# Kernel optimization log

Measured on AMD Instinct MI355X. Metric: run time of the kernel, lower is better.

Reference implementation:

```python
import jax, jax.numpy as jnp
import numpy as np
from jax import lax

GRID_SIZE = 3
SPLINE_ORDER = 2
GRID_MIN, GRID_MAX = -1.0, 1.0
KH = KW = 4
STRIDE = 2
PAD = 1
OUT_CH = 8


def _grid():
    # extended knot vector: grid_size + 2*spline_order + 1 points over [-1,1]
    h = (GRID_MAX - GRID_MIN) / GRID_SIZE
    return (jnp.arange(-SPLINE_ORDER, GRID_SIZE + SPLINE_ORDER + 1, dtype=jnp.float32) * h
            + GRID_MIN)  # [8]


def _b_splines(x, grid):
    # x: [N, F] -> bases: [N, F, GRID_SIZE + SPLINE_ORDER] via Cox-de Boor
    x = x[..., None]  # [N, F, 1]
    bases = ((x >= grid[:-1]) & (x < grid[1:])).astype(x.dtype)
    for k in range(1, SPLINE_ORDER + 1):
        left = (x - grid[: -(k + 1)]) / (grid[k:-1] - grid[: -(k + 1)]) * bases[..., :-1]
        right = (grid[k + 1:] - x) / (grid[k + 1:] - grid[1:-k]) * bases[..., 1:]
        bases = left + right
    return bases  # [N, F, 5]


def setup_inputs() -> dict:
    key = jax.random.key(0)
    ks = jax.random.split(key, 5)
    B = 2048
    x = jax.random.normal(ks[0], (B, 3, 32, 32), dtype=jnp.float32)
    F = 3 * KH * KW  # 48
    base_weight = jax.random.normal(ks[1], (OUT_CH, F), dtype=jnp.float32) * 0.1
    spline_weight = jax.random.normal(ks[2], (OUT_CH, F, GRID_SIZE + SPLINE_ORDER), dtype=jnp.float32) * 0.1
    lin_w = jax.random.normal(ks[3], (1, OUT_CH), dtype=jnp.float32) * 0.3
    lin_b = jax.random.normal(ks[4], (1,), dtype=jnp.float32) * 0.1
    return {"x": x, "base_weight": base_weight, "spline_weight": spline_weight,
            "lin_w": lin_w, "lin_b": lin_b}


def reference(x, base_weight, spline_weight, lin_w, lin_b):
    B = x.shape[0]
    grid = _grid()
    # unfold: [B, C*KH*KW, Ho, Wo], feature order (C, kh, kw) like torch.unfold
    patches = lax.conv_general_dilated_patches(
        x, (KH, KW), (STRIDE, STRIDE), ((PAD, PAD), (PAD, PAD)))
    Bp, F, Ho, Wo = patches.shape
    p = patches.transpose(0, 2, 3, 1).reshape(-1, F)  # [B*Ho*Wo, 48]
    # KANLinear: base branch + spline branch
    base = jnp.einsum('nf,of->no', jax.nn.relu(p), base_weight)
    bas = _b_splines(p, grid)  # [N, F, 5]
    spl = jnp.einsum('nfk,ofk->no', bas, spline_weight)
    y = (base + spl).reshape(B, Ho, Wo, OUT_CH)  # conv output, channels-last
    pooled = y.mean(axis=(1, 2))  # AdaptiveAvgPool2d(1) + Flatten -> [B, 8]
    out = jax.nn.sigmoid(pooled @ lin_w.T + lin_b)  # [B, 1]
    return out
```

## Files before the change

kernel.cpp:

```cpp
#include <hip/hip_runtime.h>
#include <math.h>


__global__ __launch_bounds__(256) void kan_pixel(
    const float* __restrict__ x,
    const float* __restrict__ bw,
    const float* __restrict__ sw,
    const float* __restrict__ lw,
    const float* __restrict__ lb,
    float* __restrict__ out)
{
  __shared__ float  Spad[480];
  __shared__ float  bwcL[48];
  __shared__ float4 P[768];
  __shared__ float4 T[768];
  __shared__ float  red[4];
  __shared__ float  corrS;

  const int tid = threadIdx.x;
  const int b = blockIdx.x;

  const float4* xg = reinterpret_cast<const float4*>(x) + (size_t)b * 768;
  float4 px0 = xg[tid];
  float4 px1 = xg[tid + 256];
  float4 px2 = xg[tid + 512];

  float l[8];
  #pragma unroll
  for (int o = 0; o < 8; ++o) l[o] = lw[o];

  for (int e = tid; e < 480; e += 256) {
    int f = e / 10, m = e - f * 10;
    float v = 0.f;
    if (m >= 2 && m < 7) {
      int k = f * 5 + (m - 2);
      #pragma unroll
      for (int o = 0; o < 8; ++o) v = fmaf(l[o], sw[o * 240 + k], v);
    }
    Spad[e] = v;
  }
  if (tid < 48) {
    float v = 0.f;
    #pragma unroll
    for (int o = 0; o < 8; ++o) v = fmaf(l[o], bw[o * 48 + tid], v);
    bwcL[tid] = v;
  }
  __syncthreads();

  #pragma unroll
  for (int k = 0; k < 3; ++k) {
    int e = tid + k * 256;
    int f = e >> 4, i2 = e & 15;
    float4 r4 = make_float4(0.f, 0.f, 0.f, 0.f);
    if (i2 != 0) {
      int j2 = i2 - 1, j = j2 >> 1;
      float d = 3.5f - (float)j;
      float s0 = Spad[f * 10 + j];
      float s1 = Spad[f * 10 + j + 1];
      float s2 = Spad[f * 10 + j + 2];
      float A = 0.5f * (s0 + s1);
      float B = s1 - s0;
      float C = 0.5f * s0 - s1 + 0.5f * s2;
      r4.x = A + d * (B + d * C);
      r4.y = 1.5f * B + 3.f * d * C + (j2 >= 7 ? bwcL[f] : 0.f);
      r4.z = 2.25f * C;
    }
    P[e] = r4;
  }
  __syncthreads();

  if (tid == 0) {
    float cs = 0.f;
    for (int f = 0; f < 48; ++f) {
      int kh = (f >> 2) & 3, kw = f & 3;
      int eh = (kh == 0 || kh == 3) ? 1 : 0;
      int ew = (kw == 0 || kw == 3) ? 1 : 0;
      float n = (float)(16 * eh + 16 * ew - (eh & ew));
      cs = fmaf(n, P[f * 16 + 8].x, cs);
    }
    corrS = cs;
  }

  #pragma unroll
  for (int k = 0; k < 3; ++k) {
    int e = tid + k * 256;
    int i2 = e & 15, g = e >> 4;
    int ccl = g & 3, rc = (g >> 2) & 3, c = g >> 4;
    int khA = (0x2011 >> (rc * 4)) & 15;
    int kwA = (0x2011 >> (ccl * 4)) & 15;
    bool hB = !(rc & 1);
    bool wB = !(ccl & 1);
    int fAA = ((c * 4 + khA) * 4 + kwA) * 16 + i2;
    float4 a = P[fAA];
    if (wB)       { float4 p = P[fAA + 32];  a.x += p.x; a.y += p.y; a.z += p.z; }
    if (hB)       { float4 p = P[fAA + 128]; a.x += p.x; a.y += p.y; a.z += p.z; }
    if (hB && wB) { float4 p = P[fAA + 160]; a.x += p.x; a.y += p.y; a.z += p.z; }
    T[e] = a;
  }
  __syncthreads();

  float s = 0.f;
  auto acc1 = [&](float v, int fb) {
    float fj = floorf(fmaf(v, 3.f, 7.f));
    fj = fminf(fmaxf(fj, -1.f), 14.f);
    int i2 = (int)fj + 1;
    float4 co = T[fb + i2];
    s = fmaf(v, fmaf(v, co.z, co.y), s + co.x);
  };
  const float4 pxa[3] = {px0, px1, px2};
  #pragma unroll
  for (int i = 0; i < 3; ++i) {
    int i4 = tid + (i << 8);
    int flat = i4 << 2;
    int c = flat >> 10;
    int rem = flat & 1023;
    int r = rem >> 5;
    int col0 = rem & 31;
    int rc = ((r & 1) << 1) + (r == 0 ? 1 : 0) + (r == 31 ? 1 : 0);
    int base = (((c << 2) | rc) << 6);
    acc1(pxa[i].x, base + ((col0 == 0) ? 16 : 0));
    acc1(pxa[i].y, base + 32);
    acc1(pxa[i].z, base);
    acc1(pxa[i].w, base + ((col0 == 28) ? 48 : 32));
  }

  #pragma unroll
  for (int off = 32; off; off >>= 1) s += __shfl_down(s, off);
  if ((tid & 63) == 0) red[tid >> 6] = s;
  __syncthreads();
  if (tid == 0) {
    float tot = (red[0] + red[1]) + (red[2] + red[3]) + corrS;
    float z = tot * (1.f / 256.f) + lb[0];
    out[b] = 1.f / (1.f + expf(-z));
  }
}

extern "C" void kernel_launch(void* const* d_in, const int* in_sizes, int n_in,
                              void* d_out, int out_size, void* d_ws, size_t ws_size,
                              hipStream_t stream) {
  const float* x  = (const float*)d_in[0];
  const float* bw = (const float*)d_in[1];
  const float* sw = (const float*)d_in[2];
  const float* lw = (const float*)d_in[3];
  const float* lb = (const float*)d_in[4];
  float* out = (float*)d_out;
  int B = in_sizes[0] / 3072;
  kan_pixel<<<B, 256, 0, stream>>>(x, bw, sw, lw, lb, out);
}
```

Before: 84.02 us.

## Build weight lookup table once in separate kernel instead of per block

Result: faster. 79.47 us (-5.4%).

```diff
diff --git a/kernel.cpp b/kernel.cpp
--- a/kernel.cpp
+++ b/kernel.cpp
@@ -2,29 +2,18 @@
 #include <math.h>
 
 
-__global__ __launch_bounds__(256) void kan_pixel(
-    const float* __restrict__ x,
+__global__ __launch_bounds__(256) void kan_build(
     const float* __restrict__ bw,
     const float* __restrict__ sw,
     const float* __restrict__ lw,
-    const float* __restrict__ lb,
-    float* __restrict__ out)
+    float* __restrict__ ws)
 {
   __shared__ float  Spad[480];
   __shared__ float  bwcL[48];
   __shared__ float4 P[768];
-  __shared__ float4 T[768];
-  __shared__ float  red[4];
-  __shared__ float  corrS;
+  __shared__ float  c48[48];
 
   const int tid = threadIdx.x;
-  const int b = blockIdx.x;
-
-  const float4* xg = reinterpret_cast<const float4*>(x) + (size_t)b * 768;
-  float4 px0 = xg[tid];
-  float4 px1 = xg[tid + 256];
-  float4 px2 = xg[tid + 512];
-
   float l[8];
   #pragma unroll
   for (int o = 0; o < 8; ++o) l[o] = lw[o];
@@ -69,18 +58,15 @@
   }
   __syncthreads();
 
-  if (tid == 0) {
-    float cs = 0.f;
-    for (int f = 0; f < 48; ++f) {
-      int kh = (f >> 2) & 3, kw = f & 3;
-      int eh = (kh == 0 || kh == 3) ? 1 : 0;
-      int ew = (kw == 0 || kw == 3) ? 1 : 0;
-      float n = (float)(16 * eh + 16 * ew - (eh & ew));
-      cs = fmaf(n, P[f * 16 + 8].x, cs);
-    }
-    corrS = cs;
+  if (tid < 48) {
+    int kh = (tid >> 2) & 3, kw = tid & 3;
+    int eh = (kh == 0 || kh == 3) ? 1 : 0;
+    int ew = (kw == 0 || kw == 3) ? 1 : 0;
+    float n = (float)(16 * eh + 16 * ew - (eh & ew));
+    c48[tid] = n * P[tid * 16 + 8].x;
   }
 
+  float4* tg = reinterpret_cast<float4*>(ws);
   #pragma unroll
   for (int k = 0; k < 3; ++k) {
     int e = tid + k * 256;
@@ -95,8 +81,37 @@
     if (wB)       { float4 p = P[fAA + 32];  a.x += p.x; a.y += p.y; a.z += p.z; }
     if (hB)       { float4 p = P[fAA + 128]; a.x += p.x; a.y += p.y; a.z += p.z; }
     if (hB && wB) { float4 p = P[fAA + 160]; a.x += p.x; a.y += p.y; a.z += p.z; }
-    T[e] = a;
+    tg[e] = a;
   }
+  __syncthreads();
+  if (tid == 0) {
+    float cs = 0.f;
+    for (int f = 0; f < 48; ++f) cs += c48[f];
+    ws[3072] = cs;
+  }
+}
+
+__global__ __launch_bounds__(256) void kan_main(
+    const float* __restrict__ x,
+    const float* __restrict__ ws,
+    const float* __restrict__ lb,
+    float* __restrict__ out)
+{
+  __shared__ float4 T[768];
+  __shared__ float  red[4];
+
+  const int tid = threadIdx.x;
+  const int b = blockIdx.x;
+
+  const float4* xg = reinterpret_cast<const float4*>(x) + (size_t)b * 768;
+  float4 px0 = xg[tid];
+  float4 px1 = xg[tid + 256];
+  float4 px2 = xg[tid + 512];
+
+  const float4* tg = reinterpret_cast<const float4*>(ws);
+  T[tid]       = tg[tid];
+  T[tid + 256] = tg[tid + 256];
+  T[tid + 512] = tg[tid + 512];
   __syncthreads();
 
   float s = 0.f;
@@ -129,7 +144,7 @@
   if ((tid & 63) == 0) red[tid >> 6] = s;
   __syncthreads();
   if (tid == 0) {
-    float tot = (red[0] + red[1]) + (red[2] + red[3]) + corrS;
+    float tot = (red[0] + red[1]) + (red[2] + red[3]) + ws[3072];
     float z = tot * (1.f / 256.f) + lb[0];
     out[b] = 1.f / (1.f + expf(-z));
   }
@@ -144,6 +159,8 @@
   const float* lw = (const float*)d_in[3];
   const float* lb = (const float*)d_in[4];
   float* out = (float*)d_out;
+  float* ws  = (float*)d_ws;
   int B = in_sizes[0] / 3072;
-  kan_pixel<<<B, 256, 0, stream>>>(x, bw, sw, lw, lb, out);
+  kan_build<<<1, 256, 0, stream>>>(bw, sw, lw, ws);
+  kan_main<<<B, 256, 0, stream>>>(x, ws, lb, out);
 }
```

## Fuse per-feature polynomial table into boundary-summed table build, drop a barrier

Applied to the files above, without the earlier changes.

Result: faster. 79.76 us (-5.1%).

```diff
diff --git a/kernel.cpp b/kernel.cpp
--- a/kernel.cpp
+++ b/kernel.cpp
@@ -2,7 +2,7 @@
 #include <math.h>
 
 
-__global__ __launch_bounds__(256) void kan_pixel(
+__global__ __launch_bounds__(256, 6) void kan_fused(
     const float* __restrict__ x,
     const float* __restrict__ bw,
     const float* __restrict__ sw,
@@ -10,12 +10,10 @@
     const float* __restrict__ lb,
     float* __restrict__ out)
 {
-  __shared__ float  Spad[480];
-  __shared__ float  bwcL[48];
-  __shared__ float4 P[768];
+  __shared__ float  S[240];
+  __shared__ float  bwc[48];
   __shared__ float4 T[768];
   __shared__ float  red[4];
-  __shared__ float  corrS;
 
   const int tid = threadIdx.x;
   const int b = blockIdx.x;
@@ -29,77 +27,66 @@
   #pragma unroll
   for (int o = 0; o < 8; ++o) l[o] = lw[o];
 
-  for (int e = tid; e < 480; e += 256) {
-    int f = e / 10, m = e - f * 10;
+  if (tid < 240) {
     float v = 0.f;
-    if (m >= 2 && m < 7) {
-      int k = f * 5 + (m - 2);
-      #pragma unroll
-      for (int o = 0; o < 8; ++o) v = fmaf(l[o], sw[o * 240 + k], v);
-    }
-    Spad[e] = v;
+    #pragma unroll
+    for (int o = 0; o < 8; ++o) v = fmaf(l[o], sw[o * 240 + tid], v);
+    S[tid] = v;
   }
   if (tid < 48) {
     float v = 0.f;
     #pragma unroll
     for (int o = 0; o < 8; ++o) v = fmaf(l[o], bw[o * 48 + tid], v);
-    bwcL[tid] = v;
+    bwc[tid] = v;
   }
   __syncthreads();
 
-  #pragma unroll
-  for (int k = 0; k < 3; ++k) {
-    int e = tid + k * 256;
-    int f = e >> 4, i2 = e & 15;
-    float4 r4 = make_float4(0.f, 0.f, 0.f, 0.f);
-    if (i2 != 0) {
-      int j2 = i2 - 1, j = j2 >> 1;
-      float d = 3.5f - (float)j;
-      float s0 = Spad[f * 10 + j];
-      float s1 = Spad[f * 10 + j + 1];
-      float s2 = Spad[f * 10 + j + 2];
-      float A = 0.5f * (s0 + s1);
-      float B = s1 - s0;
-      float C = 0.5f * s0 - s1 + 0.5f * s2;
-      r4.x = A + d * (B + d * C);
-      r4.y = 1.5f * B + 3.f * d * C + (j2 >= 7 ? bwcL[f] : 0.f);
-      r4.z = 2.25f * C;
-    }
-    P[e] = r4;
-  }
-  __syncthreads();
-
-  if (tid == 0) {
-    float cs = 0.f;
-    for (int f = 0; f < 48; ++f) {
-      int kh = (f >> 2) & 3, kw = f & 3;
-      int eh = (kh == 0 || kh == 3) ? 1 : 0;
-      int ew = (kw == 0 || kw == 3) ? 1 : 0;
-      float n = (float)(16 * eh + 16 * ew - (eh & ew));
-      cs = fmaf(n, P[f * 16 + 8].x, cs);
-    }
-    corrS = cs;
-  }
+  auto peval = [&](int f, int i2, float& pa, float& pb, float& pc) {
+    int j2 = i2 - 1;
+    int j  = j2 >> 1;
+    float d = 3.5f - (float)j;
+    int k0 = j - 2, k1 = j - 1, k2 = j;
+    int c0 = min(max(k0, 0), 4), c1 = min(max(k1, 0), 4), c2 = min(max(k2, 0), 4);
+    float s0 = S[f * 5 + c0]; s0 = (k0 == c0) ? s0 : 0.f;
+    float s1 = S[f * 5 + c1]; s1 = (k1 == c1) ? s1 : 0.f;
+    float s2 = S[f * 5 + c2]; s2 = (k2 == c2) ? s2 : 0.f;
+    float A = 0.5f * (s0 + s1);
+    float B = s1 - s0;
+    float C = 0.5f * s0 - s1 + 0.5f * s2;
+    pa = A + d * (B + d * C);
+    pb = 1.5f * B + 3.f * d * C + (j2 >= 7 ? bwc[f] : 0.f);
+    pc = 2.25f * C;
+  };
 
   #pragma unroll
   for (int k = 0; k < 3; ++k) {
-    int e = tid + k * 256;
+    int e = tid + (k << 8);
     int i2 = e & 15, g = e >> 4;
     int ccl = g & 3, rc = (g >> 2) & 3, c = g >> 4;
     int khA = (0x2011 >> (rc * 4)) & 15;
     int kwA = (0x2011 >> (ccl * 4)) & 15;
     bool hB = !(rc & 1);
     bool wB = !(ccl & 1);
-    int fAA = ((c * 4 + khA) * 4 + kwA) * 16 + i2;
-    float4 a = P[fAA];
-    if (wB)       { float4 p = P[fAA + 32];  a.x += p.x; a.y += p.y; a.z += p.z; }
-    if (hB)       { float4 p = P[fAA + 128]; a.x += p.x; a.y += p.y; a.z += p.z; }
-    if (hB && wB) { float4 p = P[fAA + 160]; a.x += p.x; a.y += p.y; a.z += p.z; }
-    T[e] = a;
+    int fA = (c * 4 + khA) * 4 + kwA;
+    float ax, bx, cx, ta, tb, tc;
+    peval(fA, i2, ax, bx, cx);
+    if (wB)       { peval(fA + 2,  i2, ta, tb, tc); ax += ta; bx += tb; cx += tc; }
+    if (hB)       { peval(fA + 8,  i2, ta, tb, tc); ax += ta; bx += tb; cx += tc; }
+    if (hB && wB) { peval(fA + 10, i2, ta, tb, tc); ax += ta; bx += tb; cx += tc; }
+    T[e] = make_float4(ax, bx, cx, 0.f);
+  }
+
+  float s = 0.f;
+  if (tid < 48) {
+    float pa, pb, pc;
+    peval(tid, 8, pa, pb, pc);
+    int kh = (tid >> 2) & 3, kw = tid & 3;
+    int eh = (kh == 0 || kh == 3) ? 1 : 0;
+    int ew = (kw == 0 || kw == 3) ? 1 : 0;
+    s = (float)(16 * eh + 16 * ew - (eh & ew)) * pa;
   }
   __syncthreads();
 
-  float s = 0.f;
   auto acc1 = [&](float v, int fb) {
     float fj = floorf(fmaf(v, 3.f, 7.f));
     fj = fminf(fmaxf(fj, -1.f), 14.f);
@@ -129,7 +116,7 @@
   if ((tid & 63) == 0) red[tid >> 6] = s;
   __syncthreads();
   if (tid == 0) {
-    float tot = (red[0] + red[1]) + (red[2] + red[3]) + corrS;
+    float tot = (red[0] + red[1]) + (red[2] + red[3]);
     float z = tot * (1.f / 256.f) + lb[0];
     out[b] = 1.f / (1.f + expf(-z));
   }
@@ -145,5 +132,5 @@
   const float* lb = (const float*)d_in[4];
   float* out = (float*)d_out;
   int B = in_sizes[0] / 3072;
-  kan_pixel<<<B, 256, 0, stream>>>(x, bw, sw, lw, lb, out);
+  kan_fused<<<B, 256, 0, stream>>>(x, bw, sw, lw, lb, out);
 }
```
